# Performance work log

Hardware: AMD Instinct MI355X
Metric: run time of the kernel (lower is better)

## Reference

```python
import jax, jax.numpy as jnp
import numpy as np
from math import sqrt

B, L, H, DK = 4, 2048, 16, 64


def setup_inputs() -> dict:
    key = jax.random.key(0)
    kq, kk, kv = jax.random.split(key, 3)
    queries = jax.random.normal(kq, (B, L, H, DK), dtype=jnp.float32)
    keys = jax.random.normal(kk, (B, L, H, DK), dtype=jnp.float32)
    values = jax.random.normal(kv, (B, L, H, DK), dtype=jnp.float32)
    return {"queries": queries, "keys": keys, "values": values}


def reference(queries, keys, values):
    # FullAttention forward: mask_flag=True, scale=None -> 1/sqrt(dk),
    # attention_dropout=0.0 (identity), output_attention=False.
    b, l, h, dk = queries.shape
    s = values.shape[1]
    scale = 1.0 / sqrt(dk)
    # scores: [B, H, L, S]
    scores = jnp.einsum('blhd,bshd->bhls', queries, keys)
    # causal mask: upper triangle (strictly above diagonal) -> -inf
    causal = jnp.triu(jnp.ones((l, s), dtype=bool), k=1)  # [L, S]
    scores = jnp.where(causal[None, None, :, :], -jnp.inf, scores)
    attn = jax.nn.softmax(scores * scale, axis=-1)
    out = jnp.einsum('bhls,bshd->blhd', attn, values)
    return out
```

## Files before the change

kernel.cpp:

```cpp
#include <hip/hip_runtime.h>
#include <hip/hip_bf16.h>
#include <cstdint>
#include <cstddef>

#define B_ 4
#define L_ 2048
#define H_ 16
#define D_ 64
#define BH_ (B_*H_)

typedef __attribute__((ext_vector_type(8))) short short8;
typedef __attribute__((ext_vector_type(4))) short short4_t;
typedef __attribute__((ext_vector_type(4))) float f32x4;

__device__ __forceinline__ short f2bf(float x) {
    union { float f; unsigned u; } v; v.f = x;
    unsigned r = v.u + 0x7fffu + ((v.u >> 16) & 1u);
    return (short)(r >> 16);
}

__device__ __forceinline__ short f2bf_rh(float x) {
    union { float f; unsigned u; } v; v.f = x;
    return (short)((v.u + 0x8000u) >> 16);
}

__device__ __forceinline__ short8 pack8(float4 a, float4 b, float sc) {
    short8 t;
    t[0] = f2bf(a.x * sc); t[1] = f2bf(a.y * sc);
    t[2] = f2bf(a.z * sc); t[3] = f2bf(a.w * sc);
    t[4] = f2bf(b.x * sc); t[5] = f2bf(b.y * sc);
    t[6] = f2bf(b.z * sc); t[7] = f2bf(b.w * sc);
    return t;
}

__device__ __forceinline__ float fast_exp2(float x) {
#if __has_builtin(__builtin_amdgcn_exp2f)
    return __builtin_amdgcn_exp2f(x);
#else
    return exp2f(x);
#endif
}

__device__ __forceinline__ void gld16(const void* g, void* l) {
    __builtin_amdgcn_global_load_lds(
        (const __attribute__((address_space(1))) void*)g,
        (__attribute__((address_space(3))) void*)l, 16, 0, 0);
}

__global__ __launch_bounds__(256) void prepack(
    const float* __restrict__ K, const float* __restrict__ V,
    short* __restrict__ Kb, short* __restrict__ Vt)
{
    const int blk = blockIdx.x;
    const int bh  = blk >> 5;
    const int s0  = (blk & 31) * 64;
    const int b   = bh >> 4, h = bh & 15;
    const int t   = threadIdx.x;
    __shared__ short Ls[64 * 72];

#pragma unroll
    for (int half = 0; half < 2; ++half) {
        const int sl = (t >> 3) + half * 32;
        const int dc = (t & 7) * 8;
        const size_t src_off = ((size_t)((b * L_ + s0 + sl) * H_ + h)) * D_ + dc;
        float4 f0 = *(const float4*)(K + src_off);
        float4 f1 = *(const float4*)(K + src_off + 4);
        *(short8*)&Kb[((size_t)bh * L_ + s0 + sl) * D_ + dc] = pack8(f0, f1, 1.0f);
        float4 g0 = *(const float4*)(V + src_off);
        float4 g1 = *(const float4*)(V + src_off + 4);
        *(short8*)&Ls[sl * 72 + dc] = pack8(g0, g1, 1.0f);
    }
    __syncthreads();
    const int d  = t >> 2;
    const int sc = (t & 3) * 16;
    short8 o0, o1;
#pragma unroll
    for (int j = 0; j < 8; ++j) o0[j] = Ls[(sc + j) * 72 + d];
#pragma unroll
    for (int j = 0; j < 8; ++j) o1[j] = Ls[(sc + 8 + j) * 72 + d];
    short* dst = Vt + ((size_t)bh * D_ + d) * L_ + s0 + sc;
    *(short8*)dst = o0;
    *(short8*)(dst + 8) = o1;
}

__global__ __launch_bounds__(256, 4) void fa_fwd2(
    const float* __restrict__ Q, const short* __restrict__ Kb,
    const short* __restrict__ Vt, float* __restrict__ O)
{
    const int tid  = threadIdx.x;
    const int wave = tid >> 6;
    const int lane = tid & 63;
    const int quad = lane >> 4;
    const int l16  = lane & 15;

    const int blk  = blockIdx.x;
    const int xcd  = blk & 7;
    const int slot = blk >> 3;
    const int bh   = xcd * 8 + (slot & 7);
    const int ip   = slot >> 3;
    const int b    = bh >> 4;
    const int h    = bh & 15;
    const int qtA  = ip;
    const int qtB  = 31 - ip;
    const int qbA  = qtA * 64;
    const int qbB  = qtB * 64;
    const int nkt  = qtB + 1;

    __shared__ short Ks[2][64 * 64];
    __shared__ short Vs[2][64 * 64];
    __shared__ short Ps[4][16 * 64];
    short* Pl = Ps[wave];

    const float scq = 0.125f * 1.44269504f;
    short8 qfA[2], qfB[2];
    {
        const float* qa = Q + ((size_t)((b * L_ + qbA + wave * 16 + l16) * H_ + h)) * D_;
        const float* qb = Q + ((size_t)((b * L_ + qbB + wave * 16 + l16) * H_ + h)) * D_;
#pragma unroll
        for (int kk = 0; kk < 2; ++kk) {
            const int d0 = kk * 32 + quad * 8;
            qfA[kk] = pack8(*(const float4*)(qa + d0), *(const float4*)(qa + d0 + 4), scq);
            qfB[kk] = pack8(*(const float4*)(qb + d0), *(const float4*)(qb + d0 + 4), scq);
        }
    }

    const short* Kg = Kb + (size_t)bh * L_ * D_;
    const short* Vg = Vt + (size_t)bh * D_ * L_;
    const int r8 = lane >> 3;
    const int g8 = ((lane & 7) ^ r8) * 8;

    f32x4 accA[4], accB[4];
#pragma unroll
    for (int c = 0; c < 4; ++c) {
        accA[c] = (f32x4){0.f, 0.f, 0.f, 0.f};
        accB[c] = (f32x4){0.f, 0.f, 0.f, 0.f};
    }
    float lsA[4] = {0.f, 0.f, 0.f, 0.f};
    float lsB[4] = {0.f, 0.f, 0.f, 0.f};

    auto stage = [&](int kt, int buf) {
#pragma unroll
        for (int half = 0; half < 2; ++half) {
            const int rbase = wave * 16 + half * 8;
            const int row   = rbase + r8;
            gld16(Kg + (size_t)(kt * 64 + row) * D_ + g8, &Ks[buf][rbase * 64]);
            gld16(Vg + (size_t)row * L_ + kt * 64 + g8, &Vs[buf][rbase * 64]);
        }
    };

    auto compute = [&](int kt, int buf, const short8* qf, int qt, f32x4* acc, float* ls) {
        f32x4 s[4];
#pragma unroll
        for (int ct = 0; ct < 4; ++ct) s[ct] = (f32x4){0.f, 0.f, 0.f, 0.f};
        __builtin_amdgcn_s_setprio(1);
#pragma unroll
        for (int kk = 0; kk < 2; ++kk) {
            const int cs = ((kk * 4 + quad) ^ (l16 & 7)) * 8;
#pragma unroll
            for (int ct = 0; ct < 4; ++ct) {
                short8 kf = *(short8*)&Ks[buf][(ct * 16 + l16) * 64 + cs];
                s[ct] = __builtin_amdgcn_mfma_f32_16x16x32_bf16(qf[kk], kf, s[ct], 0, 0, 0);
            }
        }
        __builtin_amdgcn_s_setprio(0);
        if (kt == qt) {
#pragma unroll
            for (int ct = 0; ct < 4; ++ct) {
#pragma unroll
                for (int r = 0; r < 4; ++r) {
                    float sv = s[ct][r];
                    if (ct * 16 + l16 > wave * 16 + quad * 4 + r) sv = -1e30f;
                    const float p = fast_exp2(sv);
                    ls[r] += p;
                    const int row = quad * 4 + r, col = ct * 16 + l16;
                    Pl[row * 64 + ((col >> 3) ^ (row & 7)) * 8 + (col & 7)] = f2bf_rh(p);
                }
            }
        } else {
#pragma unroll
            for (int ct = 0; ct < 4; ++ct) {
#pragma unroll
                for (int r = 0; r < 4; ++r) {
                    const float p = fast_exp2(s[ct][r]);
                    ls[r] += p;
                    const int row = quad * 4 + r, col = ct * 16 + l16;
                    Pl[row * 64 + ((col >> 3) ^ (row & 7)) * 8 + (col & 7)] = f2bf_rh(p);
                }
            }
        }
        __builtin_amdgcn_s_setprio(1);
#pragma unroll
        for (int ks = 0; ks < 2; ++ks) {
            const int cs = ((ks * 4 + quad) ^ (l16 & 7)) * 8;
            short8 pa = *(short8*)&Pl[l16 * 64 + cs];
#pragma unroll
            for (int cd = 0; cd < 4; ++cd) {
                short8 vb = *(short8*)&Vs[buf][(cd * 16 + l16) * 64 + cs];
                acc[cd] = __builtin_amdgcn_mfma_f32_16x16x32_bf16(pa, vb, acc[cd], 0, 0, 0);
            }
        }
        __builtin_amdgcn_s_setprio(0);
    };

    stage(0, 0);
    __syncthreads();
    for (int kt = 0; kt < nkt; ++kt) {
        const int buf = kt & 1;
        if (kt + 1 < nkt) stage(kt + 1, buf ^ 1);
        if (kt <= qtA) compute(kt, buf, qfA, qtA, accA, lsA);
        compute(kt, buf, qfB, qtB, accB, lsB);
        __syncthreads();
    }

    auto epi = [&](int qbX, f32x4* acc, float* ls) {
#pragma unroll
        for (int r = 0; r < 4; ++r) {
            float t = ls[r];
#pragma unroll
            for (int off = 1; off < 16; off <<= 1) t += __shfl_xor(t, off);
            const float inv = 1.0f / t;
            float* orow = O + ((size_t)((b * L_ + qbX + wave * 16 + quad * 4 + r) * H_ + h)) * D_ + l16;
#pragma unroll
            for (int cd = 0; cd < 4; ++cd) orow[cd * 16] = acc[cd][r] * inv;
        }
    };
    epi(qbA, accA, lsA);
    epi(qbB, accB, lsB);
}

constexpr int KS = 72;
constexpr int VS = 72;
constexpr int PS = 68;

__global__ __launch_bounds__(256) void fa_fwd(
    const float* __restrict__ Q, const float* __restrict__ K,
    const float* __restrict__ V, float* __restrict__ O)
{
    const int tid  = threadIdx.x;
    const int wave = tid >> 6;
    const int lane = tid & 63;
    const int quad = lane >> 4;
    const int l16  = lane & 15;

    const int blk  = blockIdx.x;
    const int xcd  = blk & 7;
    const int slot = blk >> 3;
    const int bh   = xcd * 8 + (slot >> 5);
    const int qtile = 31 - (slot & 31);
    const int h = bh % H_;
    const int b = bh / H_;
    const int qbase = qtile * 64;
    const int qw    = qbase + wave * 16;

    __shared__ short Ks_s[64 * KS];
    __shared__ short Vt_s[64 * VS];
    __shared__ short Ps_s[4 * 16 * PS];
    short* Pl = &Ps_s[wave * 16 * PS];

    const float* qrow = Q + ((size_t)(b * L_ + qw + l16) * H_ + h) * D_;
    short8 qf[2];
#pragma unroll
    for (int kk = 0; kk < 2; ++kk) {
        const int d0 = kk * 32 + quad * 8;
        float4 f0 = *(const float4*)(qrow + d0);
        float4 f1 = *(const float4*)(qrow + d0 + 4);
        qf[kk] = pack8(f0, f1, 0.125f * 1.44269504f);
    }

    const int ksrow = tid >> 3;
    const int kscg  = (tid & 7) * 8;
    const int vs0   = (tid >> 4) * 4;
    const int vc0   = (tid & 15) * 4;

    f32x4 acc[4];
#pragma unroll
    for (int c = 0; c < 4; ++c) acc[c] = (f32x4){0.f, 0.f, 0.f, 0.f};
    float lsum[4] = {0.f, 0.f, 0.f, 0.f};

    const int nkt = qbase / 64 + 1;

    for (int kt = 0; kt < nkt; ++kt) {
        const int kbase = kt * 64;
        __syncthreads();
#pragma unroll
        for (int half = 0; half < 2; ++half) {
            const int row = ksrow + half * 32;
            const float* kr = K + ((size_t)(b * L_ + kbase + row) * H_ + h) * D_ + kscg;
            float4 f0 = *(const float4*)kr;
            float4 f1 = *(const float4*)(kr + 4);
            *(short8*)&Ks_s[row * KS + kscg] = pack8(f0, f1, 1.0f);
        }
        {
            const float* vb0 = V + ((size_t)(b * L_ + kbase + vs0) * H_ + h) * D_ + vc0;
            float4 r0 = *(const float4*)(vb0);
            float4 r1 = *(const float4*)(vb0 + H_ * D_);
            float4 r2 = *(const float4*)(vb0 + 2 * H_ * D_);
            float4 r3 = *(const float4*)(vb0 + 3 * H_ * D_);
            short4_t w;
            w[0] = f2bf(r0.x); w[1] = f2bf(r1.x); w[2] = f2bf(r2.x); w[3] = f2bf(r3.x);
            *(short4_t*)&Vt_s[(vc0 + 0) * VS + vs0] = w;
            w[0] = f2bf(r0.y); w[1] = f2bf(r1.y); w[2] = f2bf(r2.y); w[3] = f2bf(r3.y);
            *(short4_t*)&Vt_s[(vc0 + 1) * VS + vs0] = w;
            w[0] = f2bf(r0.z); w[1] = f2bf(r1.z); w[2] = f2bf(r2.z); w[3] = f2bf(r3.z);
            *(short4_t*)&Vt_s[(vc0 + 2) * VS + vs0] = w;
            w[0] = f2bf(r0.w); w[1] = f2bf(r1.w); w[2] = f2bf(r2.w); w[3] = f2bf(r3.w);
            *(short4_t*)&Vt_s[(vc0 + 3) * VS + vs0] = w;
        }
        __syncthreads();

        f32x4 s[4];
#pragma unroll
        for (int ct = 0; ct < 4; ++ct) s[ct] = (f32x4){0.f, 0.f, 0.f, 0.f};
#pragma unroll
        for (int kk = 0; kk < 2; ++kk) {
#pragma unroll
            for (int ct = 0; ct < 4; ++ct) {
                short8 kf = *(short8*)&Ks_s[(ct * 16 + l16) * KS + kk * 32 + quad * 8];
                s[ct] = __builtin_amdgcn_mfma_f32_16x16x32_bf16(qf[kk], kf, s[ct], 0, 0, 0);
            }
        }
        const bool diag = (kbase == qbase);
#pragma unroll
        for (int ct = 0; ct < 4; ++ct) {
#pragma unroll
            for (int r = 0; r < 4; ++r) {
                float sv = s[ct][r];
                if (diag && (ct * 16 + l16 > wave * 16 + quad * 4 + r)) sv = -1e30f;
                float p = fast_exp2(sv);
                lsum[r] += p;
                Pl[(quad * 4 + r) * PS + ct * 16 + l16] = f2bf(p);
            }
        }
#pragma unroll
        for (int ks = 0; ks < 2; ++ks) {
            short8 pa = *(short8*)&Pl[l16 * PS + ks * 32 + quad * 8];
#pragma unroll
            for (int c = 0; c < 4; ++c) {
                short8 vb = *(short8*)&Vt_s[(c * 16 + l16) * VS + ks * 32 + quad * 8];
                acc[c] = __builtin_amdgcn_mfma_f32_16x16x32_bf16(pa, vb, acc[c], 0, 0, 0);
            }
        }
    }

#pragma unroll
    for (int r = 0; r < 4; ++r) {
        float t = lsum[r];
#pragma unroll
        for (int off = 1; off < 16; off <<= 1) t += __shfl_xor(t, off);
        const float inv = 1.0f / t;
        const size_t row_off = ((size_t)(b * L_ + qw + quad * 4 + r) * H_ + h) * D_;
#pragma unroll
        for (int c = 0; c < 4; ++c)
            O[row_off + c * 16 + l16] = acc[c][r] * inv;
    }
}

extern "C" void kernel_launch(void* const* d_in, const int* in_sizes, int n_in,
                              void* d_out, int out_size, void* d_ws, size_t ws_size,
                              hipStream_t stream) {
    const float* Q = (const float*)d_in[0];
    const float* K = (const float*)d_in[1];
    const float* V = (const float*)d_in[2];
    float* O = (float*)d_out;
    const size_t need = (size_t)2 * BH_ * L_ * D_ * sizeof(short);
    if (ws_size >= need) {
        short* Kb = (short*)d_ws;
        short* Vt = Kb + (size_t)BH_ * L_ * D_;
        prepack<<<dim3(BH_ * (L_ / 64)), dim3(256), 0, stream>>>(K, V, Kb, Vt);
        fa_fwd2<<<dim3(1024), dim3(256), 0, stream>>>(Q, Kb, Vt, O);
    } else {
        fa_fwd<<<dim3(B_ * H_ * (L_ / 64)), dim3(256), 0, stream>>>(Q, K, V, O);
    }
}
```

Measured before the change: 190.2 us.

## Read K/V fragments directly from global and drop paired query-tile scheduling

Removes the double-buffered LDS staging of K and V (global_load_lds plus block barriers). Each wave now loads its MFMA operands for K and the transposed V straight from global memory. It also replaces the paired light/heavy query-tile scheme with one query tile per block, launching 2048 blocks ordered heaviest-first. This removes barrier and LDS traffic, but the four waves of a block now each fetch the same K/V tiles, and V rows are read with a large stride, so cache and memory traffic rise.

After: 362.6 us. 90.7% more time.

```diff
diff --git a/kernel.cpp b/kernel.cpp
--- a/kernel.cpp
+++ b/kernel.cpp
@@ -39,12 +39,6 @@
 #else
     return exp2f(x);
 #endif
-}
-
-__device__ __forceinline__ void gld16(const void* g, void* l) {
-    __builtin_amdgcn_global_load_lds(
-        (const __attribute__((address_space(1))) void*)g,
-        (__attribute__((address_space(3))) void*)l, 16, 0, 0);
 }
 
 __global__ __launch_bounds__(256) void prepack(
@@ -97,68 +91,47 @@
     const int xcd  = blk & 7;
     const int slot = blk >> 3;
     const int bh   = xcd * 8 + (slot & 7);
-    const int ip   = slot >> 3;
+    const int qt   = 31 - (slot >> 3);
     const int b    = bh >> 4;
     const int h    = bh & 15;
-    const int qtA  = ip;
-    const int qtB  = 31 - ip;
-    const int qbA  = qtA * 64;
-    const int qbB  = qtB * 64;
-    const int nkt  = qtB + 1;
-
-    __shared__ short Ks[2][64 * 64];
-    __shared__ short Vs[2][64 * 64];
+    const int qbase = qt * 64;
+    const int qw    = qbase + wave * 16;
+    const int nkt   = qt + 1;
+
     __shared__ short Ps[4][16 * 64];
     short* Pl = Ps[wave];
 
     const float scq = 0.125f * 1.44269504f;
-    short8 qfA[2], qfB[2];
+    short8 qf[2];
     {
-        const float* qa = Q + ((size_t)((b * L_ + qbA + wave * 16 + l16) * H_ + h)) * D_;
-        const float* qb = Q + ((size_t)((b * L_ + qbB + wave * 16 + l16) * H_ + h)) * D_;
+        const float* qa = Q + ((size_t)((b * L_ + qw + l16) * H_ + h)) * D_;
 #pragma unroll
         for (int kk = 0; kk < 2; ++kk) {
             const int d0 = kk * 32 + quad * 8;
-            qfA[kk] = pack8(*(const float4*)(qa + d0), *(const float4*)(qa + d0 + 4), scq);
-            qfB[kk] = pack8(*(const float4*)(qb + d0), *(const float4*)(qb + d0 + 4), scq);
+            qf[kk] = pack8(*(const float4*)(qa + d0), *(const float4*)(qa + d0 + 4), scq);
         }
     }
 
     const short* Kg = Kb + (size_t)bh * L_ * D_;
     const short* Vg = Vt + (size_t)bh * D_ * L_;
-    const int r8 = lane >> 3;
-    const int g8 = ((lane & 7) ^ r8) * 8;
-
-    f32x4 accA[4], accB[4];
-#pragma unroll
-    for (int c = 0; c < 4; ++c) {
-        accA[c] = (f32x4){0.f, 0.f, 0.f, 0.f};
-        accB[c] = (f32x4){0.f, 0.f, 0.f, 0.f};
-    }
-    float lsA[4] = {0.f, 0.f, 0.f, 0.f};
-    float lsB[4] = {0.f, 0.f, 0.f, 0.f};
-
-    auto stage = [&](int kt, int buf) {
-#pragma unroll
-        for (int half = 0; half < 2; ++half) {
-            const int rbase = wave * 16 + half * 8;
-            const int row   = rbase + r8;
-            gld16(Kg + (size_t)(kt * 64 + row) * D_ + g8, &Ks[buf][rbase * 64]);
-            gld16(Vg + (size_t)row * L_ + kt * 64 + g8, &Vs[buf][rbase * 64]);
-        }
-    };
-
-    auto compute = [&](int kt, int buf, const short8* qf, int qt, f32x4* acc, float* ls) {
+
+    f32x4 acc[4];
+#pragma unroll
+    for (int c = 0; c < 4; ++c) acc[c] = (f32x4){0.f, 0.f, 0.f, 0.f};
+    float ls[4] = {0.f, 0.f, 0.f, 0.f};
+
+    for (int kt = 0; kt < nkt; ++kt) {
+        const short* Kt = Kg + (size_t)kt * 64 * D_;
+        const short* Vk = Vg + kt * 64;
         f32x4 s[4];
 #pragma unroll
         for (int ct = 0; ct < 4; ++ct) s[ct] = (f32x4){0.f, 0.f, 0.f, 0.f};
         __builtin_amdgcn_s_setprio(1);
 #pragma unroll
         for (int kk = 0; kk < 2; ++kk) {
-            const int cs = ((kk * 4 + quad) ^ (l16 & 7)) * 8;
 #pragma unroll
             for (int ct = 0; ct < 4; ++ct) {
-                short8 kf = *(short8*)&Ks[buf][(ct * 16 + l16) * 64 + cs];
+                short8 kf = *(const short8*)(Kt + (ct * 16 + l16) * 64 + kk * 32 + quad * 8);
                 s[ct] = __builtin_amdgcn_mfma_f32_16x16x32_bf16(qf[kk], kf, s[ct], 0, 0, 0);
             }
         }
@@ -195,37 +168,23 @@
             short8 pa = *(short8*)&Pl[l16 * 64 + cs];
 #pragma unroll
             for (int cd = 0; cd < 4; ++cd) {
-                short8 vb = *(short8*)&Vs[buf][(cd * 16 + l16) * 64 + cs];
+                short8 vb = *(const short8*)(Vk + (size_t)(cd * 16 + l16) * L_ + ks * 32 + quad * 8);
                 acc[cd] = __builtin_amdgcn_mfma_f32_16x16x32_bf16(pa, vb, acc[cd], 0, 0, 0);
             }
         }
         __builtin_amdgcn_s_setprio(0);
-    };
-
-    stage(0, 0);
-    __syncthreads();
-    for (int kt = 0; kt < nkt; ++kt) {
-        const int buf = kt & 1;
-        if (kt + 1 < nkt) stage(kt + 1, buf ^ 1);
-        if (kt <= qtA) compute(kt, buf, qfA, qtA, accA, lsA);
-        compute(kt, buf, qfB, qtB, accB, lsB);
-        __syncthreads();
-    }
-
-    auto epi = [&](int qbX, f32x4* acc, float* ls) {
-#pragma unroll
-        for (int r = 0; r < 4; ++r) {
-            float t = ls[r];
-#pragma unroll
-            for (int off = 1; off < 16; off <<= 1) t += __shfl_xor(t, off);
-            const float inv = 1.0f / t;
-            float* orow = O + ((size_t)((b * L_ + qbX + wave * 16 + quad * 4 + r) * H_ + h)) * D_ + l16;
-#pragma unroll
-            for (int cd = 0; cd < 4; ++cd) orow[cd * 16] = acc[cd][r] * inv;
-        }
-    };
-    epi(qbA, accA, lsA);
-    epi(qbB, accB, lsB);
+    }
+
+#pragma unroll
+    for (int r = 0; r < 4; ++r) {
+        float t = ls[r];
+#pragma unroll
+        for (int off = 1; off < 16; off <<= 1) t += __shfl_xor(t, off);
+        const float inv = 1.0f / t;
+        float* orow = O + ((size_t)((b * L_ + qw + quad * 4 + r) * H_ + h)) * D_ + l16;
+#pragma unroll
+        for (int cd = 0; cd < 4; ++cd) orow[cd * 16] = acc[cd][r] * inv;
+    }
 }
 
 constexpr int KS = 72;
@@ -367,7 +326,7 @@
         short* Kb = (short*)d_ws;
         short* Vt = Kb + (size_t)BH_ * L_ * D_;
         prepack<<<dim3(BH_ * (L_ / 64)), dim3(256), 0, stream>>>(K, V, Kb, Vt);
-        fa_fwd2<<<dim3(1024), dim3(256), 0, stream>>>(Q, Kb, Vt, O);
+        fa_fwd2<<<dim3(2048), dim3(256), 0, stream>>>(Q, Kb, Vt, O);
     } else {
         fa_fwd<<<dim3(B_ * H_ * (L_ / 64)), dim3(256), 0, stream>>>(Q, K, V, O);
     }
```
